# Kernel tuning notes

Measured on AMD Instinct MI355X. Metric: run time of the kernel, lower is better.

Reference implementation:

```python
import jax, jax.numpy as jnp
import numpy as np

NUM_USERS = 100000
NUM_ITEMS = 150000
N_NODES = NUM_USERS + NUM_ITEMS
LATENT_DIM = 64
N_LAYERS = 3
N_EDGES = 2000000
EPS = 0.2
CL_LAYER = 0


def setup_inputs() -> dict:
    key = jax.random.key(0)
    k1, k2, k3, k4, k5, k6 = jax.random.split(key, 6)
    user_emb = 0.1 * jax.random.normal(k1, (NUM_USERS, LATENT_DIM), dtype=jnp.float32)
    item_emb = 0.1 * jax.random.normal(k2, (NUM_ITEMS, LATENT_DIM), dtype=jnp.float32)
    vals = jax.random.uniform(k3, (N_EDGES,), dtype=jnp.float32)
    noise = jax.random.uniform(k4, (N_LAYERS, N_NODES, LATENT_DIM), dtype=jnp.float32)
    src = jax.random.randint(k5, (N_EDGES,), 0, N_NODES, dtype=jnp.int32)
    dst = jax.random.randint(k6, (N_EDGES,), 0, N_NODES, dtype=jnp.int32)
    return {"user_emb": user_emb, "item_emb": item_emb, "vals": vals,
            "noise": noise, "src": src, "dst": dst}


def _l2norm(x, axis=-1):
    return x * jax.lax.rsqrt(jnp.maximum(jnp.sum(x * x, axis=axis, keepdims=True), 1e-24))


def reference(user_emb, item_emb, vals, noise, src, dst):
    # all_emb: [N, d]
    all_emb = jnp.concatenate([user_emb, item_emb], axis=0)
    acc = all_emb  # running sum over layer outputs (layer 0 = input)
    cl_emb = all_emb
    for k in range(N_LAYERS):
        # sparse adjacency propagation: out[dst] += vals * emb[src]
        msg = vals[:, None] * all_emb[src]  # [E, d]
        all_emb = jax.ops.segment_sum(msg, dst, num_segments=N_NODES)
        # XSimGCL uniform-noise perturbation: emb += sign(emb) * normalize(noise) * eps
        all_emb = all_emb + jnp.sign(all_emb) * _l2norm(noise[k]) * EPS
        acc = acc + all_emb
        if k == CL_LAYER:
            cl_emb = all_emb
    light_out = acc / (N_LAYERS + 1)  # mean over stacked layer embeddings
    users, items = light_out[:NUM_USERS], light_out[NUM_USERS:]
    users_cl, items_cl = cl_emb[:NUM_USERS], cl_emb[NUM_USERS:]
    # norm_emb=True -> L2-normalize all outputs
    users = _l2norm(users)
    items = _l2norm(items)
    users_cl = _l2norm(users_cl)
    items_cl = _l2norm(items_cl)
    return (users, items, users_cl, items_cl)
```

## Files before the change

kernel.cpp:

```cpp
#include <hip/hip_runtime.h>

#define NUM_USERS 100000
#define NUM_ITEMS 150000
#define N_NODES   250000
#define DIM       64
#define N_EDGES   2000000
#define EPS       0.2

#define SCAN_BS 1024
#define SCAN_NB ((N_NODES + SCAN_BS - 1) / SCAN_BS)

__global__ void hist_kernel(const int* __restrict__ dst, int* __restrict__ counts) {
    int e = blockIdx.x * blockDim.x + threadIdx.x;
    if (e >= N_EDGES) return;
    atomicAdd(&counts[dst[e]], 1);
}

__global__ void scan_block(int* __restrict__ data, int* __restrict__ bsums) {
    __shared__ int tmp[SCAN_BS];
    int gid = blockIdx.x * SCAN_BS + threadIdx.x;
    int v = (gid < N_NODES) ? data[gid] : 0;
    tmp[threadIdx.x] = v;
    __syncthreads();
    for (int off = 1; off < SCAN_BS; off <<= 1) {
        int t = (threadIdx.x >= off) ? tmp[threadIdx.x - off] : 0;
        __syncthreads();
        tmp[threadIdx.x] += t;
        __syncthreads();
    }
    if (gid < N_NODES) data[gid] = tmp[threadIdx.x];
    if (threadIdx.x == SCAN_BS - 1) bsums[blockIdx.x] = tmp[SCAN_BS - 1];
}

__global__ void scan_finalize(const int* __restrict__ incl, const int* __restrict__ bsums,
                              int* __restrict__ row_ptr, int* __restrict__ cursor) {
    __shared__ int sbase[SCAN_NB];
    int tid = threadIdx.x;
    if (tid < 64) {
        int idx = tid * 4;
        int v0 = (idx + 0 < SCAN_NB) ? bsums[idx + 0] : 0;
        int v1 = (idx + 1 < SCAN_NB) ? bsums[idx + 1] : 0;
        int v2 = (idx + 2 < SCAN_NB) ? bsums[idx + 2] : 0;
        int v3 = (idx + 3 < SCAN_NB) ? bsums[idx + 3] : 0;
        int lsum = v0 + v1 + v2 + v3;
        int inc = lsum;
        #pragma unroll
        for (int off = 1; off < 64; off <<= 1) {
            int t = __shfl_up(inc, off);
            if (tid >= off) inc += t;
        }
        int base = inc - lsum;
        if (idx + 0 < SCAN_NB) sbase[idx + 0] = base;            base += v0;
        if (idx + 1 < SCAN_NB) sbase[idx + 1] = base;            base += v1;
        if (idx + 2 < SCAN_NB) sbase[idx + 2] = base;            base += v2;
        if (idx + 3 < SCAN_NB) sbase[idx + 3] = base;
    }
    __syncthreads();
    int gid = blockIdx.x * SCAN_BS + tid;
    if (gid < N_NODES) {
        int e = incl[gid] + sbase[gid >> 10];
        row_ptr[gid + 1] = e;
        if (gid + 1 < N_NODES) cursor[gid + 1] = e;
    }
    if (gid == 0) { row_ptr[0] = 0; cursor[0] = 0; }
}

__global__ void fill_kernel(const int* __restrict__ src, const int* __restrict__ dst,
                            const float* __restrict__ vals,
                            int* __restrict__ cursor, int2* __restrict__ edges) {
    int e = blockIdx.x * blockDim.x + threadIdx.x;
    if (e >= N_EDGES) return;
    int pos = atomicAdd(&cursor[dst[e]], 1);
    edges[pos] = make_int2(src[e], __float_as_int(vals[e]));
}

template<int MODE>
__global__ __launch_bounds__(256) void layer_kernel(
        const float* __restrict__ Ain,
        float* __restrict__ Aout,
        const float* __restrict__ Bprev,
        const int* __restrict__ row_ptr,
        const int2* __restrict__ edges,
        const float* __restrict__ noise,
        const float* __restrict__ userp,
        const float* __restrict__ itemp,
        float* __restrict__ out,
        float* __restrict__ cl_out) {
    int node = blockIdx.x * 4 + (threadIdx.x >> 6);
    int lane = threadIdx.x & 63;
    if (node >= N_NODES) return;
    int base = node * DIM + lane;

    const float* itemS = itemp - (size_t)NUM_USERS * DIM;

    int beg = __builtin_amdgcn_readfirstlane(row_ptr[node]);
    int end = __builtin_amdgcn_readfirstlane(row_ptr[node + 1]);

    double s0 = 0.0, s1 = 0.0, s2 = 0.0, s3 = 0.0;

    auto G = [&](int sIdx, int vbits) -> double {
        const float* b = (MODE == 0) ? ((sIdx < NUM_USERS) ? userp : itemS) : Ain;
        unsigned off = ((unsigned)sIdx << 6) + (unsigned)lane;
        return (double)__int_as_float(vbits) * (double)b[off];
    };

    int j = beg;
    if ((j & 1) && j < end) {
        int2 e = edges[j];
        s0 += G(e.x, e.y);
        ++j;
    }
    const int4* e4 = (const int4*)edges;
    int p = j >> 1;
    for (; j + 7 < end; j += 8, p += 4) {
        int4 a = e4[p], b = e4[p + 1], c = e4[p + 2], d = e4[p + 3];
        s0 += G(a.x, a.y);
        s1 += G(a.z, a.w);
        s2 += G(b.x, b.y);
        s3 += G(b.z, b.w);
        s0 += G(c.x, c.y);
        s1 += G(c.z, c.w);
        s2 += G(d.x, d.y);
        s3 += G(d.z, d.w);
    }
    for (; j + 1 < end; j += 2, ++p) {
        int4 a = e4[p];
        s0 += G(a.x, a.y);
        s1 += G(a.z, a.w);
    }
    if (j < end) {
        int2 e = edges[j];
        s0 += G(e.x, e.y);
    }
    double seg = (s0 + s1) + (s2 + s3);

    float nzf = __builtin_nontemporal_load(noise + base);
    float ssf = nzf * nzf;
    #pragma unroll
    for (int off = 32; off; off >>= 1) ssf += __shfl_xor(ssf, off);
    double nrm = (double)(nzf * (1.0f / sqrtf(fmaxf(ssf, 1e-24f))));

    double sg = (seg > 0.0) ? 1.0 : ((seg < 0.0) ? -1.0 : 0.0);
    double ne = seg + sg * nrm * EPS;

    if (MODE != 2) Aout[base] = (float)ne;

    if (MODE == 0) {
        float nef = (float)ne;
        float s2f = nef * nef;
        #pragma unroll
        for (int off = 32; off; off >>= 1) s2f += __shfl_xor(s2f, off);
        __builtin_nontemporal_store(nef * (1.0f / sqrtf(fmaxf(s2f, 1e-24f))),
                                    cl_out + base);
    }

    if (MODE == 2) {
        float e0 = (node < NUM_USERS) ? userp[base] : itemS[base];
        double a = (double)e0 + (double)Bprev[base] + (double)Ain[base] + ne;
        float af = (float)a;
        float s3f = af * af;
        #pragma unroll
        for (int off = 32; off; off >>= 1) s3f += __shfl_xor(s3f, off);
        __builtin_nontemporal_store(af * (1.0f / sqrtf(fmaxf(s3f, 1e-24f))),
                                    out + base);
    }
}

extern "C" void kernel_launch(void* const* d_in, const int* in_sizes, int n_in,
                              void* d_out, int out_size, void* d_ws, size_t ws_size,
                              hipStream_t stream) {
    const float* user  = (const float*)d_in[0];
    const float* item  = (const float*)d_in[1];
    const float* vals  = (const float*)d_in[2];
    const float* noise = (const float*)d_in[3];
    const int*   src   = (const int*)d_in[4];
    const int*   dst   = (const int*)d_in[5];

    float* out = (float*)d_out;
    float* acc = out;
    float* cl  = out + (long long)N_NODES * DIM;

    char* p = (char*)d_ws;
    float* B1 = (float*)p;  p += (size_t)N_NODES * DIM * sizeof(float);
    float* B2 = (float*)p;  p += (size_t)N_NODES * DIM * sizeof(float);
    int* row_ptr = (int*)p;   p += ((size_t)(N_NODES + 1) * 4 + 255) & ~255ull;
    int* fill    = (int*)p;   p += ((size_t)N_NODES * 4 + 255) & ~255ull;
    int* bsums   = (int*)p;   p += 4096;
    int2* edges  = (int2*)p;

    const int edgeBlocks = (N_EDGES + 255) / 256;

    hipMemsetAsync(fill, 0, (size_t)N_NODES * 4, stream);
    hist_kernel<<<edgeBlocks, 256, 0, stream>>>(dst, fill);
    scan_block<<<SCAN_NB, SCAN_BS, 0, stream>>>(fill, bsums);
    scan_finalize<<<SCAN_NB, SCAN_BS, 0, stream>>>(fill, bsums, row_ptr, fill);
    fill_kernel<<<edgeBlocks, 256, 0, stream>>>(src, dst, vals, fill, edges);

    const int layerBlocks = (N_NODES + 3) / 4;
    const float* n0 = noise;
    const float* n1 = noise + (long long)N_NODES * DIM;
    const float* n2 = noise + 2LL * N_NODES * DIM;
    layer_kernel<0><<<layerBlocks, 256, 0, stream>>>(nullptr, B1, nullptr, row_ptr, edges,
                                                     n0, user, item, nullptr, cl);
    layer_kernel<1><<<layerBlocks, 256, 0, stream>>>(B1, B2, nullptr, row_ptr, edges,
                                                     n1, user, item, nullptr, nullptr);
    layer_kernel<2><<<layerBlocks, 256, 0, stream>>>(B2, nullptr, B1, row_ptr, edges,
                                                     n2, user, item, acc, nullptr);
}
```

Measured before the change: 898.2 us.

## Build CSR via two-level bucket sort with shared-memory atomics

Replaces the global-atomic histogram, multi-kernel scan and scattered fill with a two-pass bucketed counting sort. Edges are first grouped into 512-node buckets using shared-memory histograms per block, then each bucket is sorted locally in shared memory to produce row_ptr and the CSR edge array. This aims to cut contended global atomics and random 8-byte scatter writes across a 16 MB array, at the cost of an extra temporary edge buffer and an extra pass over the edges. Local bit packing assumes src fits in 18 bits.

New measurement: 767.0 us. 1.17x faster.

```diff
diff --git a/kernel.cpp b/kernel.cpp
--- a/kernel.cpp
+++ b/kernel.cpp
@@ -7,71 +7,119 @@
 #define N_EDGES   2000000
 #define EPS       0.2
 
-#define SCAN_BS 1024
-#define SCAN_NB ((N_NODES + SCAN_BS - 1) / SCAN_BS)
-
-__global__ void hist_kernel(const int* __restrict__ dst, int* __restrict__ counts) {
-    int e = blockIdx.x * blockDim.x + threadIdx.x;
-    if (e >= N_EDGES) return;
-    atomicAdd(&counts[dst[e]], 1);
-}
-
-__global__ void scan_block(int* __restrict__ data, int* __restrict__ bsums) {
-    __shared__ int tmp[SCAN_BS];
-    int gid = blockIdx.x * SCAN_BS + threadIdx.x;
-    int v = (gid < N_NODES) ? data[gid] : 0;
-    tmp[threadIdx.x] = v;
-    __syncthreads();
-    for (int off = 1; off < SCAN_BS; off <<= 1) {
-        int t = (threadIdx.x >= off) ? tmp[threadIdx.x - off] : 0;
-        __syncthreads();
-        tmp[threadIdx.x] += t;
-        __syncthreads();
-    }
-    if (gid < N_NODES) data[gid] = tmp[threadIdx.x];
-    if (threadIdx.x == SCAN_BS - 1) bsums[blockIdx.x] = tmp[SCAN_BS - 1];
-}
-
-__global__ void scan_finalize(const int* __restrict__ incl, const int* __restrict__ bsums,
-                              int* __restrict__ row_ptr, int* __restrict__ cursor) {
-    __shared__ int sbase[SCAN_NB];
-    int tid = threadIdx.x;
-    if (tid < 64) {
-        int idx = tid * 4;
-        int v0 = (idx + 0 < SCAN_NB) ? bsums[idx + 0] : 0;
-        int v1 = (idx + 1 < SCAN_NB) ? bsums[idx + 1] : 0;
-        int v2 = (idx + 2 < SCAN_NB) ? bsums[idx + 2] : 0;
-        int v3 = (idx + 3 < SCAN_NB) ? bsums[idx + 3] : 0;
-        int lsum = v0 + v1 + v2 + v3;
+#define BK_SHIFT  9
+#define BK_NODES  512
+#define NBK       ((N_NODES + BK_NODES - 1) / BK_NODES)
+#define CNT_BLOCKS 256
+#define CNT_TILE  ((N_EDGES + CNT_BLOCKS - 1) / CNT_BLOCKS)
+
+__global__ __launch_bounds__(256) void bucket_count(const int* __restrict__ dst,
+                                                    int* __restrict__ bcnt) {
+    __shared__ int h[NBK];
+    for (int i = threadIdx.x; i < NBK; i += 256) h[i] = 0;
+    __syncthreads();
+    int start = blockIdx.x * CNT_TILE;
+    int end   = min(start + CNT_TILE, N_EDGES);
+    for (int e = start + threadIdx.x; e < end; e += 256)
+        atomicAdd(&h[dst[e] >> BK_SHIFT], 1);
+    __syncthreads();
+    for (int i = threadIdx.x; i < NBK; i += 256) {
+        int v = h[i];
+        if (v) atomicAdd(&bcnt[i], v);
+    }
+}
+
+__global__ void bucket_scan(const int* __restrict__ bcnt,
+                            int* __restrict__ bptr, int* __restrict__ bcur) {
+    int lane = threadIdx.x;
+    int idx = lane * 8;
+    int v[8]; int lsum = 0;
+    #pragma unroll
+    for (int k = 0; k < 8; ++k) { v[k] = (idx + k < NBK) ? bcnt[idx + k] : 0; lsum += v[k]; }
+    int inc = lsum;
+    #pragma unroll
+    for (int off = 1; off < 64; off <<= 1) {
+        int t = __shfl_up(inc, off);
+        if (lane >= off) inc += t;
+    }
+    int base = inc - lsum;
+    #pragma unroll
+    for (int k = 0; k < 8; ++k) {
+        if (idx + k < NBK) { bptr[idx + k] = base; bcur[idx + k] = base; }
+        base += v[k];
+    }
+    if (lane == 63) bptr[NBK] = base;
+}
+
+__global__ __launch_bounds__(256) void bucket_scatter(const int* __restrict__ src,
+                                                      const int* __restrict__ dst,
+                                                      const float* __restrict__ vals,
+                                                      int* __restrict__ bcur,
+                                                      int2* __restrict__ tmp) {
+    __shared__ int h[NBK];
+    for (int i = threadIdx.x; i < NBK; i += 256) h[i] = 0;
+    __syncthreads();
+    int start = blockIdx.x * CNT_TILE;
+    int end   = min(start + CNT_TILE, N_EDGES);
+    for (int e = start + threadIdx.x; e < end; e += 256)
+        atomicAdd(&h[dst[e] >> BK_SHIFT], 1);
+    __syncthreads();
+    for (int i = threadIdx.x; i < NBK; i += 256) {
+        int v = h[i];
+        h[i] = v ? atomicAdd(&bcur[i], v) : 0;
+    }
+    __syncthreads();
+    for (int e = start + threadIdx.x; e < end; e += 256) {
+        int d = dst[e];
+        int slot = atomicAdd(&h[d >> BK_SHIFT], 1);
+        tmp[slot] = make_int2(src[e] | ((d & (BK_NODES - 1)) << 18),
+                              __float_as_int(vals[e]));
+    }
+}
+
+__global__ __launch_bounds__(256) void bucket_build(const int2* __restrict__ tmp,
+                                                    const int* __restrict__ bptr,
+                                                    int* __restrict__ row_ptr,
+                                                    int2* __restrict__ edges) {
+    int b = blockIdx.x;
+    int s = bptr[b], e = bptr[b + 1];
+    __shared__ int cnt[BK_NODES];
+    __shared__ int off[BK_NODES];
+    for (int i = threadIdx.x; i < BK_NODES; i += 256) cnt[i] = 0;
+    __syncthreads();
+    for (int k = s + threadIdx.x; k < e; k += 256)
+        atomicAdd(&cnt[tmp[k].x >> 18], 1);
+    __syncthreads();
+    if (threadIdx.x < 64) {
+        int lane = threadIdx.x;
+        int idx = lane * 8;
+        int v[8]; int lsum = 0;
+        #pragma unroll
+        for (int k = 0; k < 8; ++k) { v[k] = cnt[idx + k]; lsum += v[k]; }
         int inc = lsum;
         #pragma unroll
-        for (int off = 1; off < 64; off <<= 1) {
-            int t = __shfl_up(inc, off);
-            if (tid >= off) inc += t;
+        for (int o = 1; o < 64; o <<= 1) {
+            int t = __shfl_up(inc, o);
+            if (lane >= o) inc += t;
         }
         int base = inc - lsum;
-        if (idx + 0 < SCAN_NB) sbase[idx + 0] = base;            base += v0;
-        if (idx + 1 < SCAN_NB) sbase[idx + 1] = base;            base += v1;
-        if (idx + 2 < SCAN_NB) sbase[idx + 2] = base;            base += v2;
-        if (idx + 3 < SCAN_NB) sbase[idx + 3] = base;
-    }
-    __syncthreads();
-    int gid = blockIdx.x * SCAN_BS + tid;
-    if (gid < N_NODES) {
-        int e = incl[gid] + sbase[gid >> 10];
-        row_ptr[gid + 1] = e;
-        if (gid + 1 < N_NODES) cursor[gid + 1] = e;
-    }
-    if (gid == 0) { row_ptr[0] = 0; cursor[0] = 0; }
-}
-
-__global__ void fill_kernel(const int* __restrict__ src, const int* __restrict__ dst,
-                            const float* __restrict__ vals,
-                            int* __restrict__ cursor, int2* __restrict__ edges) {
-    int e = blockIdx.x * blockDim.x + threadIdx.x;
-    if (e >= N_EDGES) return;
-    int pos = atomicAdd(&cursor[dst[e]], 1);
-    edges[pos] = make_int2(src[e], __float_as_int(vals[e]));
+        #pragma unroll
+        for (int k = 0; k < 8; ++k) { off[idx + k] = base; base += v[k]; }
+    }
+    __syncthreads();
+    for (int i = threadIdx.x; i < BK_NODES; i += 256) {
+        int g = (b << BK_SHIFT) + i;
+        if (g < N_NODES) row_ptr[g] = s + off[i];
+        cnt[i] = off[i];
+    }
+    if (b == 0 && threadIdx.x == 0) row_ptr[N_NODES] = N_EDGES;
+    __syncthreads();
+    for (int k = s + threadIdx.x; k < e; k += 256) {
+        int2 t = tmp[k];
+        int loc = t.x >> 18;
+        int pos = atomicAdd(&cnt[loc], 1);
+        edges[s + pos] = make_int2(t.x & 0x3FFFF, t.y);
+    }
 }
 
 template<int MODE>
@@ -184,17 +232,17 @@
     float* B1 = (float*)p;  p += (size_t)N_NODES * DIM * sizeof(float);
     float* B2 = (float*)p;  p += (size_t)N_NODES * DIM * sizeof(float);
     int* row_ptr = (int*)p;   p += ((size_t)(N_NODES + 1) * 4 + 255) & ~255ull;
-    int* fill    = (int*)p;   p += ((size_t)N_NODES * 4 + 255) & ~255ull;
-    int* bsums   = (int*)p;   p += 4096;
+    int* bcnt    = (int*)p;   p += 2048;
+    int* bptr    = (int*)p;   p += 2048;
+    int* bcur    = (int*)p;   p += 2048;
+    int2* tmp    = (int2*)p;  p += (size_t)N_EDGES * 8;
     int2* edges  = (int2*)p;
 
-    const int edgeBlocks = (N_EDGES + 255) / 256;
-
-    hipMemsetAsync(fill, 0, (size_t)N_NODES * 4, stream);
-    hist_kernel<<<edgeBlocks, 256, 0, stream>>>(dst, fill);
-    scan_block<<<SCAN_NB, SCAN_BS, 0, stream>>>(fill, bsums);
-    scan_finalize<<<SCAN_NB, SCAN_BS, 0, stream>>>(fill, bsums, row_ptr, fill);
-    fill_kernel<<<edgeBlocks, 256, 0, stream>>>(src, dst, vals, fill, edges);
+    hipMemsetAsync(bcnt, 0, NBK * sizeof(int), stream);
+    bucket_count  <<<CNT_BLOCKS, 256, 0, stream>>>(dst, bcnt);
+    bucket_scan   <<<1, 64, 0, stream>>>(bcnt, bptr, bcur);
+    bucket_scatter<<<CNT_BLOCKS, 256, 0, stream>>>(src, dst, vals, bcur, tmp);
+    bucket_build  <<<NBK, 256, 0, stream>>>(tmp, bptr, row_ptr, edges);
 
     const int layerBlocks = (N_NODES + 3) / 4;
     const float* n0 = noise;
```
